# Optimization experiments

Hardware: AMD Instinct MI355X
Metric: run time of the kernel (lower is better)

Reference implementation:

```python
import jax, jax.numpy as jnp
from jax import lax
import numpy as np

K = 3  # kernel size per dim, dimension=6 -> 3**6 = 729 taps
OFFS = np.stack(np.meshgrid(*([np.arange(K)] * 6), indexing='ij'), axis=-1).reshape(-1, 6).astype(np.int32)


def conv6d(x, kernel):
    """Dense emulation of a 1->1 channel MinkowskiConvolution over 6 spatial dims.

    x: (b, s, s, d, d, d, d) with zeros at absent sparse coordinates.
    kernel: (729,) flattened 3^6 kernel (in=out=1 channel, no bias).
    Zeros at absent coordinates contribute nothing to the gathered sums, so the
    dense conv equals the sparse conv evaluated everywhere.
    """
    xp = jnp.pad(x, [(0, 0)] + [(1, 1)] * 6)
    offs = jnp.asarray(OFFS)
    zero = jnp.int32(0)

    def body(acc, ow):
        off, wt = ow
        sl = lax.dynamic_slice(
            xp, (zero, off[0], off[1], off[2], off[3], off[4], off[5]), x.shape)
        return acc + wt * sl, None

    acc, _ = lax.scan(jax.checkpoint(body), jnp.zeros_like(x), (offs, kernel))
    return acc


def _transpose6d(t):
    # swap the two scale dims and the two image-coordinate pairs:
    # (b, s1, s2, h1, w1, h2, w2) -> (b, s2, s1, h2, w2, h1, w1)
    return jnp.transpose(t, (0, 2, 1, 5, 6, 3, 4))


def setup_inputs() -> dict:
    key = jax.random.key(0)
    k1, k2 = jax.random.split(key)
    x = jax.random.normal(k1, (1, 2, 2, 32, 32, 32, 32), dtype=jnp.float32)
    kernel = jax.random.normal(k2, (K ** 6,), dtype=jnp.float32) * 0.05
    return {"x": x, "kernel": kernel}


def reference(x, kernel):
    # MinkowskiConvolution outputs at the input coordinate set; MinkowskiSigmoid
    # acts on features at those coordinates; to_dense() zero-fills elsewhere.
    # Dense equivalent: mask to the input nonzero set.
    mask = (x != 0).astype(x.dtype)
    branch = lambda z: jax.nn.sigmoid(conv6d(jax.nn.relu(z), kernel))
    # symmetric mode: conv(x) + T(conv(T(x))); T(coords(T(x))) == coords(x)
    y = mask * (branch(x) + _transpose6d(branch(_transpose6d(x))))
    b, s1, s2, d1, d2, d3, d4 = y.shape
    y = y.reshape(b, s1 * s2, d1, d2, d3, d4).sum(axis=1)  # (b, h1, w1, h2, w2)
    return y
```

## Files before the change

### kernel.cpp

```cpp
#include <hip/hip_runtime.h>

typedef _Float16 half8 __attribute__((ext_vector_type(8)));
typedef float f16v __attribute__((ext_vector_type(16)));
typedef float f4 __attribute__((ext_vector_type(4)));
typedef unsigned long long ull;

#define X_SLAB   1048576
#define PLANE_BYTES (34*36*4*2)
#define RPT_SITES (34*34*34*36)
#define RPT_OFF  32768
#define RPT_SLACK 4096
#define TAB_ELEMS  (4*81*8)
#define OB_STRIDE 1032

__global__ __launch_bounds__(256)
void prep(const float* __restrict__ x, const float* __restrict__ w,
          ull* __restrict__ rpt, _Float16* __restrict__ tabm) {
    unsigned s = blockIdx.x * 256 + threadIdx.x;
    if (s < RPT_SITES) {
        unsigned q = s;
        int j4 = q % 36; q /= 36;
        int j3 = q % 34; q /= 34;
        int j2 = q % 34; q /= 34;
        int j1 = q;
        union { _Float16 h[4]; ull u; } pk;
        pk.u = 0ull;
        if (j1 >= 1 && j1 <= 32 && j2 >= 1 && j2 <= 32 &&
            j3 >= 1 && j3 <= 32 && j4 >= 1 && j4 <= 32) {
            size_t off = (size_t)(j1-1)*32768 + (j2-1)*1024 + (j3-1)*32 + (j4-1);
            #pragma unroll
            for (int t = 0; t < 4; ++t)
                pk.h[t] = (_Float16)fmaxf(x[(size_t)t*X_SLAB + off], 0.f);
        }
        rpt[s] = pk.u;
    }
    if (blockIdx.x == 0) {
        for (int idx = threadIdx.x; idx < 27*512; idx += 256) {
            int j = idx & 7, l = (idx >> 3) & 63, slice = idx >> 9;
            int k = 8*(l>>5) + j;
            int n = l & 31;
            int p5h = k >> 2, t = k & 3;
            float val = 0.f;
            if (n < 8 && p5h < 3) {
                int p4 = slice % 3, p3 = (slice/3) % 3, p2 = slice/9;
                int br = n & 1, sc = n >> 1, s1 = sc >> 1, s2 = sc & 1;
                int t1 = t >> 1, t2 = t & 1;
                int a = t1 - s1 + 1, b = t2 - s2 + 1;
                int widx = (br == 0)
                    ? (a*243 + b*81 + p2*27 + p3*9 + p4*3 + p5h)
                    : (b*243 + a*81 + p4*27 + p5h*9 + p2*3 + p3);
                val = w[widx];
            }
            tabm[idx] = (_Float16)val;
        }
    }
}

__global__ __launch_bounds__(256)
void conv_mfma(const float* __restrict__ x, const ull* __restrict__ rpt,
               const _Float16* __restrict__ tabm, float* __restrict__ out) {
    __shared__ __align__(16) unsigned char arena[34048];
    _Float16* planeh = (_Float16*)arena;
    float*    obuf   = (float*)arena;
    unsigned char* msk = arena + 33024;

    const int tid  = threadIdx.x;
    const int lane = tid & 63;
    const int wv   = tid >> 6;
    const int e2 = blockIdx.x, e1 = blockIdx.y;
    const size_t blockbase = (size_t)e1*32768 + (size_t)e2*1024;

    {
        int p = tid * 4;
        f4 a0 = *(const f4*)(x + 0*(size_t)X_SLAB + blockbase + p);
        f4 a1 = *(const f4*)(x + 1*(size_t)X_SLAB + blockbase + p);
        f4 a2 = *(const f4*)(x + 2*(size_t)X_SLAB + blockbase + p);
        f4 a3 = *(const f4*)(x + 3*(size_t)X_SLAB + blockbase + p);
        #pragma unroll
        for (int q = 0; q < 4; ++q) {
            unsigned b = (a0[q] != 0.f ? 1u : 0u) | (a1[q] != 0.f ? 2u : 0u)
                       | (a2[q] != 0.f ? 4u : 0u) | (a3[q] != 0.f ? 8u : 0u);
            msk[p + q] = (unsigned char)b;
        }
    }

    f16v acc[8];
    #pragma unroll
    for (int r = 0; r < 8; ++r)
        #pragma unroll
        for (int i = 0; i < 16; ++i) acc[r][i] = 0.f;

    const int R   = wv * 8;
    const int j4b = (lane & 31) + 2*(lane >> 5);

    #pragma unroll 1
    for (int p2 = 0; p2 < 3; ++p2) {
        #pragma unroll 1
        for (int p3 = 0; p3 < 3; ++p3) {
            const char* pgb = (const char*)rpt
                            + ((size_t)(e1+p2)*34 + (e2+p3)) * PLANE_BYTES;
            __syncthreads();
            #pragma unroll
            for (int kk = 0; kk < 3; ++kk) {
                int off = (tid + kk*256) * 16;
                __builtin_amdgcn_global_load_lds(
                    (const __attribute__((address_space(1))) unsigned int*)(pgb + off),
                    (__attribute__((address_space(3))) unsigned int*)(arena + off),
                    16, 0, 0);
            }
            __syncthreads();

            const int sb = ((p2*3 + p3)*3) * 512;
            half8 B0 = *(const half8*)(tabm + sb          + lane*8);
            half8 B1 = *(const half8*)(tabm + sb +  512   + lane*8);
            half8 B2 = *(const half8*)(tabm + sb + 1024   + lane*8);

            #pragma unroll
            for (int j3l = 0; j3l < 10; ++j3l) {
                const ull* ap = (const ull*)(planeh + ((R + j3l)*36 + j4b)*4);
                union { ull u[2]; half8 h; } A;
                A.u[0] = ap[0]; A.u[1] = ap[1];
                if (j3l <= 7)
                    acc[j3l]   = __builtin_amdgcn_mfma_f32_32x32x16_f16(A.h, B0, acc[j3l],   0,0,0);
                if (j3l >= 1 && j3l <= 8)
                    acc[j3l-1] = __builtin_amdgcn_mfma_f32_32x32x16_f16(A.h, B1, acc[j3l-1], 0,0,0);
                if (j3l >= 2)
                    acc[j3l-2] = __builtin_amdgcn_mfma_f32_32x32x16_f16(A.h, B2, acc[j3l-2], 0,0,0);
            }
        }
    }

    __syncthreads();
    {
        const int n   = lane & 31;
        const int mb4 = 4*(lane >> 5);
        if (n < 8) {
            #pragma unroll
            for (int rloc = 0; rloc < 8; ++rloc) {
                #pragma unroll
                for (int g = 0; g < 4; ++g) {
                    f4 v;
                    v.x = acc[rloc][4*g+0]; v.y = acc[rloc][4*g+1];
                    v.z = acc[rloc][4*g+2]; v.w = acc[rloc][4*g+3];
                    int point = (R + rloc)*32 + 8*g + mb4;
                    *(f4*)&obuf[n*OB_STRIDE + point] = v;
                }
            }
        }
    }
    __syncthreads();
    {
        int p0 = tid * 4;
        f4 vals[8];
        #pragma unroll
        for (int n = 0; n < 8; ++n)
            vals[n] = *(const f4*)&obuf[n*OB_STRIDE + p0];
        unsigned mword = *(const unsigned*)&msk[p0];
        f4 r4;
        #pragma unroll
        for (int q = 0; q < 4; ++q) {
            unsigned nib = (mword >> (8*q)) & 0xFu;
            float res = 0.f;
            #pragma unroll
            for (int i = 0; i < 4; ++i) {
                float s0 = __builtin_amdgcn_rcpf(1.f + __expf(-vals[2*i][q]));
                float s1 = __builtin_amdgcn_rcpf(1.f + __expf(-vals[2*i+1][q]));
                float m  = ((nib >> i) & 1u) ? 1.f : 0.f;
                res = fmaf(m, s0 + s1, res);
            }
            r4[q] = res;
        }
        *(f4*)(out + blockbase + p0) = r4;
    }
}

__global__ void build_wtab(const float* __restrict__ w, float* __restrict__ tab) {
    int idx = blockIdx.x * blockDim.x + threadIdx.x;
    if (idx >= TAB_ELEMS) return;
    int n  = idx & 7;
    int r  = idx >> 3;
    int p5 = r % 3; r /= 3;
    int p4 = r % 3; r /= 3;
    int p3 = r % 3; r /= 3;
    int p2 = r % 3; r /= 3;
    int t  = r;
    int t1 = t >> 1, t2 = t & 1;
    int br = n & 1;
    int s  = n >> 1;
    int s1 = s >> 1, s2 = s & 1;
    int a = t1 - s1 + 1;
    int b = t2 - s2 + 1;
    int widx = (br == 0)
        ? (a*243 + b*81 + p2*27 + p3*9 + p4*3 + p5)
        : (b*243 + a*81 + p4*27 + p5*9 + p2*3 + p3);
    tab[idx] = w[widx];
}

__global__ __launch_bounds__(256)
void conv_fp32(const float* __restrict__ x,
               const float* __restrict__ tab,
               float* __restrict__ out) {
    const int e4 = threadIdx.x;
    const int e3 = blockIdx.x * 8 + threadIdx.y;
    const int e2 = blockIdx.y;
    const int e1 = blockIdx.z;

    float acc[8];
    #pragma unroll
    for (int n = 0; n < 8; ++n) acc[n] = 0.f;

    #pragma unroll 1
    for (int t = 0; t < 4; ++t) {
        const float* st  = x + (size_t)t * X_SLAB;
        const float* wt0 = tab + t * 648;
        #pragma unroll
        for (int p2 = 0; p2 < 3; ++p2) {
            #pragma unroll
            for (int p3 = 0; p3 < 3; ++p3) {
                int i1 = e1 + p2 - 1, i2 = e2 + p3 - 1;
                bool v12 = ((unsigned)i1 < 32u) && ((unsigned)i2 < 32u);
                const float* base = st + (i1*32768 + i2*1024 + (e3-1)*32 + (e4-1));
                const float* wt = wt0 + (p2*3 + p3) * 72;
                #pragma unroll
                for (int p4 = 0; p4 < 3; ++p4) {
                    int i3 = e3 + p4 - 1;
                    bool v3 = v12 && ((unsigned)i3 < 32u);
                    #pragma unroll
                    for (int p5 = 0; p5 < 3; ++p5) {
                        int i4 = e4 + p5 - 1;
                        bool ok = v3 && ((unsigned)i4 < 32u);
                        float v = ok ? fmaxf(base[p4*32 + p5], 0.f) : 0.f;
                        const float* w8 = wt + (p4*3 + p5)*8;
                        #pragma unroll
                        for (int n = 0; n < 8; ++n)
                            acc[n] = fmaf(w8[n], v, acc[n]);
                    }
                }
            }
        }
    }

    const size_t eflat = (size_t)e1*32768 + e2*1024 + e3*32 + e4;
    float res = 0.f;
    #pragma unroll
    for (int i = 0; i < 4; ++i) {
        float xv = x[(size_t)i * X_SLAB + eflat];
        float s0 = __builtin_amdgcn_rcpf(1.f + __expf(-acc[2*i]));
        float s1 = __builtin_amdgcn_rcpf(1.f + __expf(-acc[2*i+1]));
        float m  = (xv != 0.f) ? 1.f : 0.f;
        res = fmaf(m, s0 + s1, res);
    }
    out[eflat] = res;
}

extern "C" void kernel_launch(void* const* d_in, const int* in_sizes, int n_in,
                              void* d_out, int out_size, void* d_ws, size_t ws_size,
                              hipStream_t stream) {
    const float* x = (const float*)d_in[0];
    const float* w = (const float*)d_in[1];
    float* out = (float*)d_out;

    const size_t need = (size_t)RPT_OFF + (size_t)RPT_SITES*8ull + RPT_SLACK;

    if (ws_size >= need) {
        _Float16* tabm = (_Float16*)d_ws;
        ull*      rpt  = (ull*)((char*)d_ws + RPT_OFF);
        prep<<<dim3((RPT_SITES + 255)/256), dim3(256), 0, stream>>>(x, w, rpt, tabm);
        dim3 grd(32, 32, 1), blk(256, 1, 1);
        conv_mfma<<<grd, blk, 0, stream>>>(x, rpt, tabm, out);
    } else {
        float* tab = (float*)d_ws;
        build_wtab<<<dim3((TAB_ELEMS + 255)/256), dim3(256), 0, stream>>>(w, tab);
        dim3 blk(32, 8, 1), grd(4, 32, 32);
        conv_fp32<<<grd, blk, 0, stream>>>(x, tab, out);
    }
}
```

Before: 106.8 us.

## Pack four e2 outputs into MFMA N dimension and double-buffer planes

Each block now computes four adjacent e2 slices at once. The 32-wide MFMA N dimension previously carried only 8 useful columns and now carries 4x8, using a weight table extended over six e2-relative plane offsets. Plane loads into LDS are double-buffered so the next plane and B fragments are fetched while the current one is multiplied. The epilogue applies sigmoid and the mask in registers and reduces across lanes with shuffles instead of staging through LDS. The grid shrinks fourfold, and each block does 18 plane iterations instead of 9.

```diff
diff --git a/kernel.cpp b/kernel.cpp
--- a/kernel.cpp
+++ b/kernel.cpp
@@ -8,10 +8,10 @@
 #define X_SLAB   1048576
 #define PLANE_BYTES (34*36*4*2)
 #define RPT_SITES (34*34*34*36)
-#define RPT_OFF  32768
+#define RPT_OFF  65536
 #define RPT_SLACK 4096
+#define TAB_N    (3*6*3*512)
 #define TAB_ELEMS  (4*81*8)
-#define OB_STRIDE 1032
 
 __global__ __launch_bounds__(256)
 void prep(const float* __restrict__ x, const float* __restrict__ w,
@@ -35,15 +35,17 @@
         rpt[s] = pk.u;
     }
     if (blockIdx.x == 0) {
-        for (int idx = threadIdx.x; idx < 27*512; idx += 256) {
+        for (int idx = threadIdx.x; idx < TAB_N; idx += 256) {
             int j = idx & 7, l = (idx >> 3) & 63, slice = idx >> 9;
+            int p4 = slice % 3, j2rel = (slice/3) % 6, p2 = slice/18;
+            int n32 = l & 31;
+            int d2 = n32 >> 3, n8 = n32 & 7;
             int k = 8*(l>>5) + j;
-            int n = l & 31;
             int p5h = k >> 2, t = k & 3;
+            int p3 = j2rel - d2;
             float val = 0.f;
-            if (n < 8 && p5h < 3) {
-                int p4 = slice % 3, p3 = (slice/3) % 3, p2 = slice/9;
-                int br = n & 1, sc = n >> 1, s1 = sc >> 1, s2 = sc & 1;
+            if (p5h < 3 && p3 >= 0 && p3 <= 2) {
+                int br = n8 & 1, sc = n8 >> 1, s1 = sc >> 1, s2 = sc & 1;
                 int t1 = t >> 1, t2 = t & 1;
                 int a = t1 - s1 + 1, b = t2 - s2 + 1;
                 int widx = (br == 0)
@@ -59,28 +61,32 @@
 __global__ __launch_bounds__(256)
 void conv_mfma(const float* __restrict__ x, const ull* __restrict__ rpt,
                const _Float16* __restrict__ tabm, float* __restrict__ out) {
-    __shared__ __align__(16) unsigned char arena[34048];
-    _Float16* planeh = (_Float16*)arena;
-    float*    obuf   = (float*)arena;
-    unsigned char* msk = arena + 33024;
+    __shared__ __align__(16) unsigned char arena[2*12288 + 4096];
+    unsigned char* msk = arena + 24576;
 
     const int tid  = threadIdx.x;
     const int lane = tid & 63;
     const int wv   = tid >> 6;
-    const int e2 = blockIdx.x, e1 = blockIdx.y;
-    const size_t blockbase = (size_t)e1*32768 + (size_t)e2*1024;
+    const int e2b  = blockIdx.x * 4;
+    const int e1   = blockIdx.y;
+    const size_t blockbase = (size_t)e1*32768 + (size_t)e2b*1024;
 
     {
-        int p = tid * 4;
-        f4 a0 = *(const f4*)(x + 0*(size_t)X_SLAB + blockbase + p);
-        f4 a1 = *(const f4*)(x + 1*(size_t)X_SLAB + blockbase + p);
-        f4 a2 = *(const f4*)(x + 2*(size_t)X_SLAB + blockbase + p);
-        f4 a3 = *(const f4*)(x + 3*(size_t)X_SLAB + blockbase + p);
-        #pragma unroll
-        for (int q = 0; q < 4; ++q) {
-            unsigned b = (a0[q] != 0.f ? 1u : 0u) | (a1[q] != 0.f ? 2u : 0u)
-                       | (a2[q] != 0.f ? 4u : 0u) | (a3[q] != 0.f ? 8u : 0u);
-            msk[p + q] = (unsigned char)b;
+        int p0 = tid * 16;
+        #pragma unroll
+        for (int g = 0; g < 4; ++g) {
+            f4 a0 = *(const f4*)(x + (size_t)0*X_SLAB + blockbase + p0 + 4*g);
+            f4 a1 = *(const f4*)(x + (size_t)1*X_SLAB + blockbase + p0 + 4*g);
+            f4 a2 = *(const f4*)(x + (size_t)2*X_SLAB + blockbase + p0 + 4*g);
+            f4 a3 = *(const f4*)(x + (size_t)3*X_SLAB + blockbase + p0 + 4*g);
+            unsigned wbits = 0;
+            #pragma unroll
+            for (int q = 0; q < 4; ++q) {
+                unsigned b = (a0[q] != 0.f ? 1u : 0u) | (a1[q] != 0.f ? 2u : 0u)
+                           | (a2[q] != 0.f ? 4u : 0u) | (a3[q] != 0.f ? 8u : 0u);
+                wbits |= b << (8*q);
+            }
+            *(unsigned*)&msk[p0 + 4*g] = wbits;
         }
     }
 
@@ -93,84 +99,94 @@
     const int R   = wv * 8;
     const int j4b = (lane & 31) + 2*(lane >> 5);
 
+    half8 Bn[3];
+    {
+        const char* pgb = (const char*)rpt + ((size_t)(e1+0)*34 + (e2b+0))*PLANE_BYTES;
+        #pragma unroll
+        for (int kk = 0; kk < 3; ++kk) {
+            int off = (tid + kk*256) * 16;
+            __builtin_amdgcn_global_load_lds(
+                (const __attribute__((address_space(1))) unsigned int*)(pgb + off),
+                (__attribute__((address_space(3))) unsigned int*)(arena + off),
+                16, 0, 0);
+        }
+        const _Float16* tb = tabm + lane*8;
+        Bn[0] = *(const half8*)(tb);
+        Bn[1] = *(const half8*)(tb + 512);
+        Bn[2] = *(const half8*)(tb + 1024);
+    }
+
     #pragma unroll 1
-    for (int p2 = 0; p2 < 3; ++p2) {
-        #pragma unroll 1
-        for (int p3 = 0; p3 < 3; ++p3) {
+    for (int it = 0; it < 18; ++it) {
+        const int buf = it & 1;
+        __syncthreads();
+        half8 B0 = Bn[0], B1 = Bn[1], B2 = Bn[2];
+        if (it + 1 < 18) {
+            const int nit = it + 1;
+            const int p2 = nit / 6, j2 = nit % 6;
             const char* pgb = (const char*)rpt
-                            + ((size_t)(e1+p2)*34 + (e2+p3)) * PLANE_BYTES;
-            __syncthreads();
+                            + ((size_t)(e1+p2)*34 + (e2b+j2)) * PLANE_BYTES;
+            char* dst = (char*)arena + (buf^1)*12288;
             #pragma unroll
             for (int kk = 0; kk < 3; ++kk) {
                 int off = (tid + kk*256) * 16;
                 __builtin_amdgcn_global_load_lds(
                     (const __attribute__((address_space(1))) unsigned int*)(pgb + off),
-                    (__attribute__((address_space(3))) unsigned int*)(arena + off),
+                    (__attribute__((address_space(3))) unsigned int*)(dst + off),
                     16, 0, 0);
             }
-            __syncthreads();
-
-            const int sb = ((p2*3 + p3)*3) * 512;
-            half8 B0 = *(const half8*)(tabm + sb          + lane*8);
-            half8 B1 = *(const half8*)(tabm + sb +  512   + lane*8);
-            half8 B2 = *(const half8*)(tabm + sb + 1024   + lane*8);
-
-            #pragma unroll
-            for (int j3l = 0; j3l < 10; ++j3l) {
-                const ull* ap = (const ull*)(planeh + ((R + j3l)*36 + j4b)*4);
-                union { ull u[2]; half8 h; } A;
-                A.u[0] = ap[0]; A.u[1] = ap[1];
-                if (j3l <= 7)
-                    acc[j3l]   = __builtin_amdgcn_mfma_f32_32x32x16_f16(A.h, B0, acc[j3l],   0,0,0);
-                if (j3l >= 1 && j3l <= 8)
-                    acc[j3l-1] = __builtin_amdgcn_mfma_f32_32x32x16_f16(A.h, B1, acc[j3l-1], 0,0,0);
-                if (j3l >= 2)
-                    acc[j3l-2] = __builtin_amdgcn_mfma_f32_32x32x16_f16(A.h, B2, acc[j3l-2], 0,0,0);
-            }
-        }
-    }
-
-    __syncthreads();
-    {
-        const int n   = lane & 31;
-        const int mb4 = 4*(lane >> 5);
-        if (n < 8) {
-            #pragma unroll
-            for (int rloc = 0; rloc < 8; ++rloc) {
-                #pragma unroll
-                for (int g = 0; g < 4; ++g) {
-                    f4 v;
-                    v.x = acc[rloc][4*g+0]; v.y = acc[rloc][4*g+1];
-                    v.z = acc[rloc][4*g+2]; v.w = acc[rloc][4*g+3];
-                    int point = (R + rloc)*32 + 8*g + mb4;
-                    *(f4*)&obuf[n*OB_STRIDE + point] = v;
-                }
-            }
-        }
-    }
-    __syncthreads();
-    {
-        int p0 = tid * 4;
-        f4 vals[8];
-        #pragma unroll
-        for (int n = 0; n < 8; ++n)
-            vals[n] = *(const f4*)&obuf[n*OB_STRIDE + p0];
-        unsigned mword = *(const unsigned*)&msk[p0];
-        f4 r4;
-        #pragma unroll
-        for (int q = 0; q < 4; ++q) {
-            unsigned nib = (mword >> (8*q)) & 0xFu;
-            float res = 0.f;
-            #pragma unroll
-            for (int i = 0; i < 4; ++i) {
-                float s0 = __builtin_amdgcn_rcpf(1.f + __expf(-vals[2*i][q]));
-                float s1 = __builtin_amdgcn_rcpf(1.f + __expf(-vals[2*i+1][q]));
-                float m  = ((nib >> i) & 1u) ? 1.f : 0.f;
-                res = fmaf(m, s0 + s1, res);
-            }
-            r4[q] = res;
-        }
-        *(f4*)(out + blockbase + p0) = r4;
+            const _Float16* tb = tabm + (size_t)nit*1536 + lane*8;
+            Bn[0] = *(const half8*)(tb);
+            Bn[1] = *(const half8*)(tb + 512);
+            Bn[2] = *(const half8*)(tb + 1024);
+        }
+        const _Float16* planeh = (const _Float16*)(arena + buf*12288);
+        #pragma unroll
+        for (int j3l = 0; j3l < 10; ++j3l) {
+            const ull* ap = (const ull*)(planeh + ((R + j3l)*36 + j4b)*4);
+            union { ull u[2]; half8 h; } A;
+            A.u[0] = ap[0]; A.u[1] = ap[1];
+            if (j3l <= 7)
+                acc[j3l]   = __builtin_amdgcn_mfma_f32_32x32x16_f16(A.h, B0, acc[j3l],   0,0,0);
+            if (j3l >= 1 && j3l <= 8)
+                acc[j3l-1] = __builtin_amdgcn_mfma_f32_32x32x16_f16(A.h, B1, acc[j3l-1], 0,0,0);
+            if (j3l >= 2)
+                acc[j3l-2] = __builtin_amdgcn_mfma_f32_32x32x16_f16(A.h, B2, acc[j3l-2], 0,0,0);
+        }
+    }
+
+    const int n8 = lane & 7;
+    const int d2 = (lane >> 3) & 3;
+    const int h  = lane >> 5;
+    const int sbit = n8 >> 1;
+    float* outp = out + blockbase + (size_t)d2*1024;
+    #pragma unroll
+    for (int rloc = 0; rloc < 8; ++rloc) {
+        const int e3 = R + rloc;
+        float v[16];
+        #pragma unroll
+        for (int g = 0; g < 4; ++g) {
+            unsigned mw = *(const unsigned*)&msk[d2*1024 + e3*32 + 8*g + 4*h];
+            #pragma unroll
+            for (int j = 0; j < 4; ++j) {
+                float a  = acc[rloc][4*g + j];
+                float sg = __builtin_amdgcn_rcpf(1.f + __expf(-a));
+                v[4*g+j] = ((mw >> (8*j + sbit)) & 1u) ? sg : 0.f;
+            }
+        }
+        #pragma unroll
+        for (int i = 0; i < 16; ++i) {
+            v[i] += __shfl_xor(v[i], 1);
+            v[i] += __shfl_xor(v[i], 2);
+            v[i] += __shfl_xor(v[i], 4);
+        }
+        if (n8 == 0) {
+            #pragma unroll
+            for (int g = 0; g < 4; ++g) {
+                f4 o; o.x = v[4*g]; o.y = v[4*g+1]; o.z = v[4*g+2]; o.w = v[4*g+3];
+                *(f4*)(outp + e3*32 + 8*g + 4*h) = o;
+            }
+        }
     }
 }
 
@@ -266,7 +282,7 @@
         _Float16* tabm = (_Float16*)d_ws;
         ull*      rpt  = (ull*)((char*)d_ws + RPT_OFF);
         prep<<<dim3((RPT_SITES + 255)/256), dim3(256), 0, stream>>>(x, w, rpt, tabm);
-        dim3 grd(32, 32, 1), blk(256, 1, 1);
+        dim3 grd(8, 32, 1), blk(256, 1, 1);
         conv_mfma<<<grd, blk, 0, stream>>>(x, rpt, tabm, out);
     } else {
         float* tab = (float*)d_ws;
```

After: 104.2 us. -2.5%, faster.
